# Performance work log

Measured on AMD Instinct MI355X. Metric: run time of the kernel, lower is better.

## Reference

```python
import jax, jax.numpy as jnp
import numpy as np
from jax import lax

T, B, NPG, F_IN = 10, 8, 1080, 2
N = B * NPG            # 8640 nodes total
DEG = 16
E = N * DEG            # 138240 edges
HID, HEADS = 64, 8
LSTM_H, OUT = 128, 2
NEG_SLOPE = 0.2

# (in_dim, heads, out_channels_per_head) for the 4 GATConv layers
LAYER_DIMS = [(F_IN, HEADS, HID), (HID * HEADS, HEADS, HID // 2),
              (HID // 2 * HEADS, HEADS, HID // 4), (HID // 4 * HEADS, 1, HID // 8)]


def setup_inputs() -> dict:
    key = jax.random.key(0)
    ks = iter(jax.random.split(key, 40))
    inp = {}
    inp['x_seq'] = jax.random.normal(next(ks), (T, N, F_IN), jnp.float32)
    # kNN-style edges within each graph: every node receives DEG random in-graph neighbors
    dst = jnp.repeat(jnp.arange(N, dtype=jnp.int32), DEG)
    offs = (dst // NPG) * NPG
    src = offs + jax.random.randint(next(ks), (E,), 0, NPG, jnp.int32)
    inp['edge_index'] = jnp.stack([src, dst])
    inp['batch'] = jnp.repeat(jnp.arange(B, dtype=jnp.int32), NPG)
    # GAT params: W [in, H*C], att_src/att_dst [H, C], bias [H*C]
    for li, (fin, h, c) in enumerate(LAYER_DIMS, start=1):
        s = 1.0 / np.sqrt(fin)
        inp[f'W{li}'] = jax.random.uniform(next(ks), (fin, h * c), jnp.float32, -s, s)
        inp[f'as{li}'] = jax.random.uniform(next(ks), (h, c), jnp.float32, -s, s)
        inp[f'ad{li}'] = jax.random.uniform(next(ks), (h, c), jnp.float32, -s, s)
        inp[f'b{li}'] = jnp.zeros((h * c,), jnp.float32)
    # LSTM (PyTorch layout, gate order i,f,g,o)
    gdim = HID // 8
    sl = 1.0 / np.sqrt(LSTM_H)
    inp['w_ih'] = jax.random.uniform(next(ks), (4 * LSTM_H, gdim), jnp.float32, -sl, sl)
    inp['w_hh'] = jax.random.uniform(next(ks), (4 * LSTM_H, LSTM_H), jnp.float32, -sl, sl)
    inp['b_ih'] = jax.random.uniform(next(ks), (4 * LSTM_H,), jnp.float32, -sl, sl)
    inp['b_hh'] = jax.random.uniform(next(ks), (4 * LSTM_H,), jnp.float32, -sl, sl)
    inp['w_fc'] = jax.random.uniform(next(ks), (OUT, LSTM_H), jnp.float32, -sl, sl)
    inp['b_fc'] = jax.random.uniform(next(ks), (OUT,), jnp.float32, -sl, sl)
    return inp


def _forward(x_seq, W1, as1, ad1, b1, W2, as2, ad2, b2, W3, as3, ad3, b3,
             W4, as4, ad4, b4, w_ih, w_hh, b_ih, b_hh, w_fc, b_fc,
             edge_index, batch):
    # PyG GATConv adds self-loops by default
    loops = jnp.arange(N, dtype=edge_index.dtype)
    src = jnp.concatenate([edge_index[0], loops])
    dst = jnp.concatenate([edge_index[1], loops])

    def gat(x, W, a_s, a_d, b):
        Hh, C = a_s.shape
        h = (x @ W).reshape(N, Hh, C)                 # [N,H,C]
        e_s = (h * a_s).sum(-1)                        # [N,H]
        e_d = (h * a_d).sum(-1)
        e = jax.nn.leaky_relu(e_s[src] + e_d[dst], NEG_SLOPE)   # [Etot,H]
        m = jax.ops.segment_max(e, dst, num_segments=N)
        ex = jnp.exp(e - m[dst])
        den = jax.ops.segment_sum(ex, dst, num_segments=N)
        alpha = ex / (den[dst] + 1e-16)
        out = jax.ops.segment_sum(h[src] * alpha[:, :, None], dst, num_segments=N)
        return out.reshape(N, Hh * C) + b

    counts = jax.ops.segment_sum(jnp.ones((N,), jnp.float32), batch, num_segments=B)[:, None]

    def per_t(x):  # eval mode: dropout = identity
        x = jax.nn.elu(gat(x, W1, as1, ad1, b1))
        x = jax.nn.elu(gat(x, W2, as2, ad2, b2))
        x = jax.nn.elu(gat(x, W3, as3, ad3, b3))
        x = jax.nn.elu(gat(x, W4, as4, ad4, b4))
        return jax.ops.segment_sum(x, batch, num_segments=B) / counts  # mean pool [B, hid//8]

    _, embs = lax.scan(lambda c, xt: (c, per_t(xt)), None, x_seq)  # [T,B,gdim]

    h0 = jnp.zeros((B, LSTM_H), x_seq.dtype)
    c0 = jnp.zeros((B, LSTM_H), x_seq.dtype)

    def step(carry, xt):
        h, c = carry
        g = xt @ w_ih.T + h @ w_hh.T + b_ih + b_hh
        i, f, gg, o = jnp.split(g, 4, axis=-1)
        c = jax.nn.sigmoid(f) * c + jax.nn.sigmoid(i) * jnp.tanh(gg)
        h = jax.nn.sigmoid(o) * jnp.tanh(c)
        return (h, c), None

    (h_last, _), _ = lax.scan(step, (h0, c0), embs)
    return h_last @ w_fc.T + b_fc  # [B, OUT] (eval path: last timestep only)


def reference(x_seq, W1, as1, ad1, b1, W2, as2, ad2, b2, W3, as3, ad3, b3,
              W4, as4, ad4, b4, w_ih, w_hh, b_ih, b_hh, w_fc, b_fc,
              edge_index, batch):
    return _forward(x_seq, W1, as1, ad1, b1, W2, as2, ad2, b2, W3, as3, ad3, b3,
                    W4, as4, ad4, b4, w_ih, w_hh, b_ih, b_hh, w_fc, b_fc,
                    edge_index, batch)
```

## Files before the change

kernel.cpp:

```cpp
#include <hip/hip_runtime.h>
#include <math.h>

#define T_TOT 10
#define NB    8
#define NPG   1080
#define NN    (NB*NPG)
#define DEG   16

typedef unsigned short ushortT;
using short8 = __attribute__((ext_vector_type(8))) short;
using f32x4  = __attribute__((ext_vector_type(4))) float;

__device__ __forceinline__ float lrelu(float v) { return v > 0.f ? v : 0.2f*v; }
__device__ __forceinline__ float elu1(float v)  { return v > 0.f ? v : (__expf(v) - 1.f); }
__device__ __forceinline__ float bf2f(ushortT h){ return __uint_as_float(((unsigned)h) << 16); }
__device__ __forceinline__ ushortT rne(float v) {
    unsigned u = __float_as_uint(v);
    u += 0x7FFFu + ((u >> 16) & 1u);
    return (ushortT)(u >> 16);
}
__device__ __forceinline__ int xswz(int b, int nwg) {
    int q = nwg >> 3, r = nwg & 7;
    int x = b & 7, i = b >> 3;
    return x*q + min(x, r) + i;
}

__global__ void k_prep_l1(const float* __restrict__ W1, const float* __restrict__ as1,
                          const float* __restrict__ ad1, float* __restrict__ A) {
    int tid = threadIdx.x;
    if (tid >= 32) return;
    int h = tid & 7, k = (tid >> 3) & 1, sd = tid >> 4;
    const float* att = sd ? ad1 : as1;
    float acc = 0.f;
    for (int c = 0; c < 64; ++c) acc += W1[k*512 + h*64 + c] * att[h*64 + c];
    A[sd*16 + k*8 + h] = acc;
}

__global__ void k_prepW(const float* __restrict__ W, ushortT* __restrict__ WT, int K, int M) {
    int i = blockIdx.x*256 + threadIdx.x;
    if (i >= K*M) return;
    int k = i / M, m = i - k*M;
    WT[(size_t)m*K + k] = rne(W[i]);
}

__global__ void k_e1(const float* __restrict__ x, const float* __restrict__ A,
                     float* __restrict__ es, float* __restrict__ ed, int R) {
    int r = blockIdx.x*256 + threadIdx.x;
    if (r >= R) return;
    float x0 = x[2*r], x1 = x[2*r+1];
    #pragma unroll
    for (int h = 0; h < 8; ++h) {
        es[r*8+h] = x0*A[h]    + x1*A[8+h];
        ed[r*8+h] = x0*A[16+h] + x1*A[24+h];
    }
}

__global__ __launch_bounds__(256) void k_gat1(
    const float* __restrict__ x, const int* __restrict__ esrc,
    const float* __restrict__ es, const float* __restrict__ ed,
    const float* __restrict__ W1, const float* __restrict__ b1,
    ushortT* __restrict__ q, int R) {
    int tid = threadIdx.x;
    int g = xswz(blockIdx.x, gridDim.x)*16 + (tid >> 4);
    int l = tid & 15;
    if (g >= R*8) g = R*8 - 1;
    int r = g >> 3, hh = g & 7;
    int t = r / NN, n = r - t*NN;
    float edv = ed[r*8 + hh];
    int s0 = t*NN + esrc[n*DEG + l];
    float e0 = lrelu(es[s0*8 + hh] + edv);
    float e1 = (l == 0) ? lrelu(es[r*8 + hh] + edv) : -1e30f;
    float m = fmaxf(e0, e1);
    #pragma unroll
    for (int off = 8; off >= 1; off >>= 1) m = fmaxf(m, __shfl_xor(m, off, 16));
    float ex0 = __expf(e0 - m);
    float ex1 = (l == 0) ? __expf(e1 - m) : 0.f;
    float den = ex0 + ex1;
    float p0 = ex0*x[2*s0]   + ex1*x[2*r];
    float p1 = ex0*x[2*s0+1] + ex1*x[2*r+1];
    #pragma unroll
    for (int off = 8; off >= 1; off >>= 1) {
        den += __shfl_xor(den, off, 16);
        p0  += __shfl_xor(p0,  off, 16);
        p1  += __shfl_xor(p1,  off, 16);
    }
    float inv = 1.f/(den + 1e-16f);
    float xa0 = p0*inv, xa1 = p1*inv;
    int col = hh*64 + l*4;
    float4 w0 = *(const float4*)&W1[col];
    float4 w1 = *(const float4*)&W1[512 + col];
    float4 bb = *(const float4*)&b1[col];
    ushort4 h4;
    h4.x = rne(elu1(xa0*w0.x + xa1*w1.x + bb.x));
    h4.y = rne(elu1(xa0*w0.y + xa1*w1.y + bb.y));
    h4.z = rne(elu1(xa0*w0.z + xa1*w1.z + bb.z));
    h4.w = rne(elu1(xa0*w0.w + xa1*w1.w + bb.w));
    *(ushort4*)&q[(size_t)r*512 + col] = h4;
}

template<int H, int C, bool BFIN, bool BFOUT>
__global__ __launch_bounds__(256) void k_gat(
    const void* __restrict__ hb_, const int* __restrict__ esrc,
    const float* __restrict__ es, const float* __restrict__ ed,
    const float* __restrict__ bias, float* __restrict__ out,
    ushortT* __restrict__ ohi, int R) {
    constexpr int LANES = C/4;
    constexpr int GPB = 256/LANES;
    constexpr int EPL = (17 + LANES - 1)/LANES;
    __shared__ float wsm[GPB][17];
    __shared__ int   ssm[GPB][17];
    int tid = threadIdx.x;
    int grp = tid / LANES;
    int l = tid % LANES;
    int g = xswz(blockIdx.x, gridDim.x)*GPB + grp;
    if (g >= R*H) g = R*H - 1;
    int r = g / H, hh = g % H;
    int t = r / NN, n = r - t*NN;
    float edv = ed[(size_t)r*H + hh];
    float ev[EPL]; int sv[EPL];
    float m = -1e30f;
    #pragma unroll
    for (int s = 0; s < EPL; ++s) {
        int j = s*LANES + l;
        if (j < 17) {
            int src = (j == 16) ? r : (t*NN + esrc[n*DEG + j]);
            sv[s] = src;
            float e = lrelu(es[(size_t)src*H + hh] + edv);
            ev[s] = e; m = fmaxf(m, e);
        } else { ev[s] = -1e30f; sv[s] = r; }
    }
    #pragma unroll
    for (int off = LANES/2; off >= 1; off >>= 1) m = fmaxf(m, __shfl_xor(m, off, LANES));
    float den = 0.f;
    #pragma unroll
    for (int s = 0; s < EPL; ++s) {
        int j = s*LANES + l;
        float e2 = (j < 17) ? __expf(ev[s] - m) : 0.f;
        ev[s] = e2; den += e2;
    }
    #pragma unroll
    for (int off = LANES/2; off >= 1; off >>= 1) den += __shfl_xor(den, off, LANES);
    float inv = 1.f/(den + 1e-16f);
    #pragma unroll
    for (int s = 0; s < EPL; ++s) {
        int j = s*LANES + l;
        if (j < 17) { wsm[grp][j] = ev[s]*inv; ssm[grp][j] = sv[s]; }
    }
    __syncthreads();
    constexpr int HC = H*C;
    int base = hh*C + l*4;
    float ax = 0.f, ay = 0.f, az = 0.f, aw = 0.f;
    #pragma unroll
    for (int j = 0; j < 17; ++j) {
        float wj = wsm[grp][j];
        if constexpr (BFIN) {
            ushort4 hv = *(const ushort4*)&((const ushortT*)hb_)[(size_t)ssm[grp][j]*HC + base];
            ax += wj*bf2f(hv.x); ay += wj*bf2f(hv.y); az += wj*bf2f(hv.z); aw += wj*bf2f(hv.w);
        } else {
            float4 hv = *(const float4*)&((const float*)hb_)[(size_t)ssm[grp][j]*HC + base];
            ax += wj*hv.x; ay += wj*hv.y; az += wj*hv.z; aw += wj*hv.w;
        }
    }
    float4 bb = *(const float4*)&bias[base];
    float vx = elu1(ax + bb.x), vy = elu1(ay + bb.y);
    float vz = elu1(az + bb.z), vw = elu1(aw + bb.w);
    if constexpr (BFOUT) {
        ushort4 h4;
        h4.x = rne(vx); h4.y = rne(vy); h4.z = rne(vz); h4.w = rne(vw);
        *(ushort4*)&ohi[(size_t)r*HC + base] = h4;
    } else {
        *(float4*)&out[(size_t)r*HC + base] = make_float4(vx, vy, vz, vw);
    }
}

template<int C>
__global__ __launch_bounds__(256) void k_gemm_mfma(
    const ushortT* __restrict__ X, const ushortT* __restrict__ WT,
    const float* __restrict__ as_, const float* __restrict__ ad_,
    ushortT* __restrict__ Hout, float* __restrict__ es, float* __restrict__ ed,
    int R, int K, int M) {
    __shared__ __align__(16) char smem[32768];
    int tid = threadIdx.x;
    int wid = tid >> 6, l = tid & 63;
    int l15 = l & 15, lg = l >> 4;
    int wr = wid >> 1, wc = wid & 1;
    int rb = blockIdx.x*128, cb = blockIdx.y*128;

    f32x4 acc[4][4] = {};
    int aoff[4], asw[4], boff[4], bsw[4];
    #pragma unroll
    for (int i = 0; i < 4; ++i) {
        int ar = wr*64 + i*16 + l15;
        aoff[i] = ar*128; asw[i] = (ar & 7) << 4;
        int bc = wc*64 + i*16 + l15;
        boff[i] = 16384 + bc*128; bsw[i] = (bc & 7) << 4;
    }
    int kb0 = lg*16;
    const size_t strideB = (size_t)K*2;
    int srow = tid >> 3, sc8 = tid & 7;
    int ssw = ((srow & 7) << 4);
    const int nKT = K >> 6;

    for (int kt = 0; kt < nKT; ++kt) {
        int kbyte = kt*128;
        __syncthreads();
        #pragma unroll
        for (int i = 0; i < 4; ++i) {
            int row = srow + i*32;
            int dst = row*128 + ((sc8*16) ^ ssw);
            int rg = min(rb + row, R - 1);
            uint4 va = *(const uint4*)((const char*)X  + (size_t)rg*strideB + kbyte + sc8*16);
            uint4 vw = *(const uint4*)((const char*)WT + (size_t)(cb + row)*strideB + kbyte + sc8*16);
            *(uint4*)(smem + dst)         = va;
            *(uint4*)(smem + 16384 + dst) = vw;
        }
        __syncthreads();
        #pragma unroll
        for (int ks = 0; ks < 2; ++ks) {
            int kb = ks*64 + kb0;
            short8 ah[4], bv[4];
            #pragma unroll
            for (int i = 0; i < 4; ++i) {
                ah[i] = *(const short8*)(smem + aoff[i] + (kb ^ asw[i]));
                bv[i] = *(const short8*)(smem + boff[i] + (kb ^ bsw[i]));
            }
            #pragma unroll
            for (int mt = 0; mt < 4; ++mt)
                #pragma unroll
                for (int nt = 0; nt < 4; ++nt)
                    acc[mt][nt] = __builtin_amdgcn_mfma_f32_16x16x32_bf16(ah[mt], bv[nt], acc[mt][nt], 0, 0, 0);
        }
    }
    __syncthreads();
    constexpr int NSL = 128/C;
    constexpr int NHW = 64/C;
    int hg0 = cb / C;
    float asv[4], adv[4];
    #pragma unroll
    for (int nt = 0; nt < 4; ++nt) {
        int col = wc*64 + nt*16 + l15;
        int h = col / C, c = col - h*C;
        asv[nt] = as_[(hg0 + h)*C + c];
        adv[nt] = ad_[(hg0 + h)*C + c];
    }
    float* ebp = (float*)smem;
    #pragma unroll
    for (int mt = 0; mt < 4; ++mt) {
        float ps[4][NHW] = {}, pd[4][NHW] = {};
        #pragma unroll
        for (int nt = 0; nt < 4; ++nt) {
            int sl = (nt*16)/C;
            #pragma unroll
            for (int q = 0; q < 4; ++q) {
                ps[q][sl] += acc[mt][nt][q]*asv[nt];
                pd[q][sl] += acc[mt][nt][q]*adv[nt];
            }
        }
        #pragma unroll
        for (int off = 1; off < 16; off <<= 1)
            #pragma unroll
            for (int q = 0; q < 4; ++q)
                #pragma unroll
                for (int sl = 0; sl < NHW; ++sl) {
                    ps[q][sl] += __shfl_xor(ps[q][sl], off);
                    pd[q][sl] += __shfl_xor(pd[q][sl], off);
                }
        if (l15 == 0) {
            #pragma unroll
            for (int q = 0; q < 4; ++q) {
                int row = wr*64 + mt*16 + lg*4 + q;
                #pragma unroll
                for (int sl = 0; sl < NHW; ++sl) {
                    ebp[(row*NSL + wc*NHW + sl)*2 + 0] = ps[q][sl];
                    ebp[(row*NSL + wc*NHW + sl)*2 + 1] = pd[q][sl];
                }
            }
        }
        #pragma unroll
        for (int nt = 0; nt < 4; ++nt) {
            int col = cb + wc*64 + nt*16 + l15;
            #pragma unroll
            for (int q = 0; q < 4; ++q) {
                int r = rb + wr*64 + mt*16 + lg*4 + q;
                if (r < R) Hout[(size_t)r*M + col] = rne(acc[mt][nt][q]);
            }
        }
    }
    __syncthreads();
    for (int i = tid; i < 128*NSL; i += 256) {
        int row = i / NSL, sl = i - row*NSL;
        int r = rb + row;
        if (r < R) {
            es[(size_t)r*8 + hg0 + sl] = ebp[i*2 + 0];
            ed[(size_t)r*8 + hg0 + sl] = ebp[i*2 + 1];
        }
    }
}

__global__ __launch_bounds__(256) void k_lin4(
    const float* __restrict__ X, const float* __restrict__ W,
    const float* __restrict__ as_, const float* __restrict__ ad_,
    float* __restrict__ Hout, float* __restrict__ es, float* __restrict__ ed, int R) {
    int tid = threadIdx.x;
    int lane = tid & 63;
    int rl = lane >> 3, cc = lane & 7;
    int r = blockIdx.x*32 + (tid >> 6)*8 + rl;
    if (r >= R) return;
    const float* xp = X + (size_t)r*128;
    float acc = 0.f;
    #pragma unroll 8
    for (int k = 0; k < 128; ++k) acc += xp[k] * W[k*8 + cc];
    Hout[(size_t)r*8 + cc] = acc;
    float ps = acc * as_[cc], pd = acc * ad_[cc];
    #pragma unroll
    for (int off = 4; off >= 1; off >>= 1) {
        ps += __shfl_xor(ps, off, 64);
        pd += __shfl_xor(pd, off, 64);
    }
    if (cc == 0) { es[r] = ps; ed[r] = pd; }
}

__global__ void k_pool(const float* __restrict__ x4, float* __restrict__ emb, int t0) {
    __shared__ float red[256];
    int tl = blockIdx.x >> 3, b = blockIdx.x & 7;
    int tid = threadIdx.x;
    int c = tid & 7, nl = tid >> 3;
    float s = 0.f;
    for (int k = 0; k < 34; ++k) {
        int n = nl + 32*k;
        if (n < NPG) s += x4[((size_t)tl*NN + b*NPG + n)*8 + c];
    }
    red[tid] = s;
    __syncthreads();
    for (int st = 16; st >= 1; st >>= 1) {
        if (nl < st) red[tid] += red[tid + st*8];
        __syncthreads();
    }
    if (nl == 0) emb[((t0 + tl)*8 + b)*8 + c] = red[c] * (1.f/1080.f);
}

__global__ __launch_bounds__(512) void k_lstm(
    const float* __restrict__ emb, const float* __restrict__ w_ih,
    const float* __restrict__ w_hh, const float* __restrict__ b_ih,
    const float* __restrict__ b_hh, const float* __restrict__ w_fc,
    const float* __restrict__ b_fc, float* __restrict__ out) {
    int b = blockIdx.x, u = threadIdx.x;
    __shared__ float h[128], cst[128], g[512], eall[T_TOT*8];
    if (u < 128) { h[u] = 0.f; cst[u] = 0.f; }
    if (u < T_TOT*8) eall[u] = emb[((u >> 3)*8 + b)*8 + (u & 7)];
    float wreg[128];
    {
        const float* wp = w_hh + (size_t)u*128;
        #pragma unroll
        for (int k4 = 0; k4 < 32; ++k4) {
            float4 v = *(const float4*)&wp[k4*4];
            wreg[4*k4+0] = v.x; wreg[4*k4+1] = v.y;
            wreg[4*k4+2] = v.z; wreg[4*k4+3] = v.w;
        }
    }
    float wih[8];
    #pragma unroll
    for (int k = 0; k < 8; ++k) wih[k] = w_ih[(size_t)u*8 + k];
    float bsum = b_ih[u] + b_hh[u];
    __syncthreads();
    for (int t = 0; t < T_TOT; ++t) {
        float a0 = bsum, a1 = 0.f, a2 = 0.f, a3 = 0.f;
        #pragma unroll
        for (int k = 0; k < 8; ++k) a0 += eall[t*8 + k]*wih[k];
        #pragma unroll
        for (int k = 0; k < 32; ++k) {
            a0 += h[4*k+0]*wreg[4*k+0];
            a1 += h[4*k+1]*wreg[4*k+1];
            a2 += h[4*k+2]*wreg[4*k+2];
            a3 += h[4*k+3]*wreg[4*k+3];
        }
        g[u] = (a0 + a1) + (a2 + a3);
        __syncthreads();
        if (u < 128) {
            float ig = 1.f/(1.f + __expf(-g[u]));
            float fg = 1.f/(1.f + __expf(-g[128+u]));
            float gg = tanhf(g[256+u]);
            float og = 1.f/(1.f + __expf(-g[384+u]));
            float cn = fg*cst[u] + ig*gg;
            cst[u] = cn;
            h[u] = og*tanhf(cn);
        }
        __syncthreads();
    }
    if (u < 64) {
        float p0 = h[u]*w_fc[u]       + h[u+64]*w_fc[64+u];
        float p1 = h[u]*w_fc[128+u]   + h[u+64]*w_fc[192+u];
        #pragma unroll
        for (int off = 32; off >= 1; off >>= 1) {
            p0 += __shfl_xor(p0, off, 64);
            p1 += __shfl_xor(p1, off, 64);
        }
        if (u == 0) {
            out[b*2 + 0] = p0 + b_fc[0];
            out[b*2 + 1] = p1 + b_fc[1];
        }
    }
}

extern "C" void kernel_launch(void* const* d_in, const int* in_sizes, int n_in,
                              void* d_out, int out_size, void* d_ws, size_t ws_size,
                              hipStream_t stream) {
    const float* x_seq = (const float*)d_in[0];
    const int*   edge  = (const int*)d_in[1];
    const float* W1 = (const float*)d_in[3];
    const float* as1 = (const float*)d_in[4];
    const float* ad1 = (const float*)d_in[5];
    const float* b1  = (const float*)d_in[6];
    const float* W2 = (const float*)d_in[7];
    const float* as2 = (const float*)d_in[8];
    const float* ad2 = (const float*)d_in[9];
    const float* b2  = (const float*)d_in[10];
    const float* W3 = (const float*)d_in[11];
    const float* as3 = (const float*)d_in[12];
    const float* ad3 = (const float*)d_in[13];
    const float* b3  = (const float*)d_in[14];
    const float* W4 = (const float*)d_in[15];
    const float* as4 = (const float*)d_in[16];
    const float* ad4 = (const float*)d_in[17];
    const float* b4  = (const float*)d_in[18];
    const float* w_ih = (const float*)d_in[19];
    const float* w_hh = (const float*)d_in[20];
    const float* b_ih = (const float*)d_in[21];
    const float* b_hh = (const float*)d_in[22];
    const float* w_fc = (const float*)d_in[23];
    const float* b_fc = (const float*)d_in[24];

    char* w = (char*)d_ws;
    auto alloc = [&](size_t bytes) {
        char* p = w; w += (bytes + 255) & ~(size_t)255; return p;
    };
    float*   A1  = (float*)alloc(128);
    float*   emb = (float*)alloc((size_t)T_TOT*8*8*4);
    ushortT* W2T = (ushortT*)alloc((size_t)256*512*2);
    ushortT* W3T = (ushortT*)alloc((size_t)128*256*2);
    size_t used = (size_t)(w - (char*)d_ws);
    size_t perT = (size_t)NN*(1024 + 512 + 512 + 256 + 512 + 128);
    size_t rem = (ws_size > used + 4096) ? ws_size - used - 4096 : 0;
    int Tc = (int)(rem / perT);
    if (Tc > T_TOT) Tc = T_TOT;
    if (Tc < 1) Tc = 1;
    ushortT* Q  = (ushortT*)alloc((size_t)Tc*NN*1024);
    ushortT* P  = (ushortT*)alloc((size_t)Tc*NN*512);
    ushortT* G3 = (ushortT*)alloc((size_t)Tc*NN*512);
    ushortT* H3 = (ushortT*)alloc((size_t)Tc*NN*256);
    float*   G4 = (float*)alloc((size_t)Tc*NN*512);
    float*   ES = (float*)alloc((size_t)Tc*NN*32);
    float*   ED = (float*)alloc((size_t)Tc*NN*32);
    float*   P4 = (float*)alloc((size_t)Tc*NN*32);
    float*   G5 = (float*)alloc((size_t)Tc*NN*32);

    k_prep_l1<<<1, 64, 0, stream>>>(W1, as1, ad1, A1);
    k_prepW<<<(256*512 + 255)/256, 256, 0, stream>>>(W2, W2T, 512, 256);
    k_prepW<<<(128*256 + 255)/256, 256, 0, stream>>>(W3, W3T, 256, 128);

    for (int t0 = 0; t0 < T_TOT; t0 += Tc) {
        int tc = (Tc < T_TOT - t0) ? Tc : (T_TOT - t0);
        int R = tc*NN;
        int nrb = (R + 127)/128;
        const float* xoff = x_seq + (size_t)t0*NN*2;
        k_e1<<<(R + 255)/256, 256, 0, stream>>>(xoff, A1, ES, ED, R);
        k_gat1<<<R/2, 256, 0, stream>>>(xoff, edge, ES, ED, W1, b1, Q, R);
        k_gemm_mfma<32><<<dim3(nrb, 2), 256, 0, stream>>>(Q, W2T, as2, ad2, P, ES, ED, R, 512, 256);
        k_gat<8,32,true,true><<<R/4, 256, 0, stream>>>(P, edge, ES, ED, b2, nullptr, G3, R);
        k_gemm_mfma<16><<<dim3(nrb, 1), 256, 0, stream>>>(G3, W3T, as3, ad3, H3, ES, ED, R, 256, 128);
        k_gat<8,16,true,false><<<R/8, 256, 0, stream>>>(H3, edge, ES, ED, b3, G4, nullptr, R);
        k_lin4<<<R/32, 256, 0, stream>>>(G4, W4, as4, ad4, P4, ES, ED, R);
        k_gat<1,8,false,false><<<(R + 127)/128, 256, 0, stream>>>(P4, edge, ES, ED, b4, G5, nullptr, R);
        k_pool<<<tc*8, 256, 0, stream>>>(G5, emb, t0);
    }
    k_lstm<<<8, 512, 0, stream>>>(emb, w_ih, w_hh, b_ih, b_hh, w_fc, b_fc, (float*)d_out);
}
```

Baseline: 437.8 us.

## Fuse layer-1 scores into gat1, widen per-lane gathers, store layer-3 output as bf16

```diff
diff --git a/kernel.cpp b/kernel.cpp
--- a/kernel.cpp
+++ b/kernel.cpp
@@ -14,10 +14,15 @@
 __device__ __forceinline__ float lrelu(float v) { return v > 0.f ? v : 0.2f*v; }
 __device__ __forceinline__ float elu1(float v)  { return v > 0.f ? v : (__expf(v) - 1.f); }
 __device__ __forceinline__ float bf2f(ushortT h){ return __uint_as_float(((unsigned)h) << 16); }
+__device__ __forceinline__ float bfl(unsigned u){ return __uint_as_float(u << 16); }
+__device__ __forceinline__ float bfh(unsigned u){ return __uint_as_float(u & 0xFFFF0000u); }
 __device__ __forceinline__ ushortT rne(float v) {
     unsigned u = __float_as_uint(v);
     u += 0x7FFFu + ((u >> 16) & 1u);
     return (ushortT)(u >> 16);
+}
+__device__ __forceinline__ unsigned pk2(float a, float b) {
+    return (unsigned)rne(a) | ((unsigned)rne(b) << 16);
 }
 __device__ __forceinline__ int xswz(int b, int nwg) {
     int q = nwg >> 3, r = nwg & 7;
@@ -43,76 +48,78 @@
     WT[(size_t)m*K + k] = rne(W[i]);
 }
 
-__global__ void k_e1(const float* __restrict__ x, const float* __restrict__ A,
-                     float* __restrict__ es, float* __restrict__ ed, int R) {
-    int r = blockIdx.x*256 + threadIdx.x;
-    if (r >= R) return;
-    float x0 = x[2*r], x1 = x[2*r+1];
-    #pragma unroll
-    for (int h = 0; h < 8; ++h) {
-        es[r*8+h] = x0*A[h]    + x1*A[8+h];
-        ed[r*8+h] = x0*A[16+h] + x1*A[24+h];
-    }
-}
-
 __global__ __launch_bounds__(256) void k_gat1(
     const float* __restrict__ x, const int* __restrict__ esrc,
-    const float* __restrict__ es, const float* __restrict__ ed,
-    const float* __restrict__ W1, const float* __restrict__ b1,
-    ushortT* __restrict__ q, int R) {
+    const float* __restrict__ A, const float* __restrict__ W1,
+    const float* __restrict__ b1, ushortT* __restrict__ q, int R) {
     int tid = threadIdx.x;
-    int g = xswz(blockIdx.x, gridDim.x)*16 + (tid >> 4);
-    int l = tid & 15;
+    int g = xswz(blockIdx.x, gridDim.x)*32 + (tid >> 3);
+    int l = tid & 7;
     if (g >= R*8) g = R*8 - 1;
     int r = g >> 3, hh = g & 7;
     int t = r / NN, n = r - t*NN;
-    float edv = ed[r*8 + hh];
-    int s0 = t*NN + esrc[n*DEG + l];
-    float e0 = lrelu(es[s0*8 + hh] + edv);
-    float e1 = (l == 0) ? lrelu(es[r*8 + hh] + edv) : -1e30f;
-    float m = fmaxf(e0, e1);
-    #pragma unroll
-    for (int off = 8; off >= 1; off >>= 1) m = fmaxf(m, __shfl_xor(m, off, 16));
-    float ex0 = __expf(e0 - m);
-    float ex1 = (l == 0) ? __expf(e1 - m) : 0.f;
-    float den = ex0 + ex1;
-    float p0 = ex0*x[2*s0]   + ex1*x[2*r];
-    float p1 = ex0*x[2*s0+1] + ex1*x[2*r+1];
-    #pragma unroll
-    for (int off = 8; off >= 1; off >>= 1) {
-        den += __shfl_xor(den, off, 16);
-        p0  += __shfl_xor(p0,  off, 16);
-        p1  += __shfl_xor(p1,  off, 16);
+    float2 xr = *(const float2*)&x[2*r];
+    float As0 = A[hh], As1 = A[8+hh];
+    float edv = xr.x*A[16+hh] + xr.y*A[24+hh];
+    float ev[3], xs0[3], xs1[3];
+    float m = -1e30f;
+    #pragma unroll
+    for (int s = 0; s < 3; ++s) {
+        int j = s*8 + l;
+        if (j < 17) {
+            int src = (j == 16) ? r : (t*NN + esrc[n*DEG + j]);
+            float2 xs = *(const float2*)&x[2*src];
+            xs0[s] = xs.x; xs1[s] = xs.y;
+            float e = lrelu(xs.x*As0 + xs.y*As1 + edv);
+            ev[s] = e; m = fmaxf(m, e);
+        } else { ev[s] = -1e30f; xs0[s] = 0.f; xs1[s] = 0.f; }
+    }
+    #pragma unroll
+    for (int off = 4; off >= 1; off >>= 1) m = fmaxf(m, __shfl_xor(m, off, 8));
+    float den = 0.f, p0 = 0.f, p1 = 0.f;
+    #pragma unroll
+    for (int s = 0; s < 3; ++s) {
+        float e2 = __expf(ev[s] - m);
+        den += e2; p0 += e2*xs0[s]; p1 += e2*xs1[s];
+    }
+    #pragma unroll
+    for (int off = 4; off >= 1; off >>= 1) {
+        den += __shfl_xor(den, off, 8);
+        p0  += __shfl_xor(p0,  off, 8);
+        p1  += __shfl_xor(p1,  off, 8);
     }
     float inv = 1.f/(den + 1e-16f);
     float xa0 = p0*inv, xa1 = p1*inv;
-    int col = hh*64 + l*4;
-    float4 w0 = *(const float4*)&W1[col];
-    float4 w1 = *(const float4*)&W1[512 + col];
-    float4 bb = *(const float4*)&b1[col];
-    ushort4 h4;
-    h4.x = rne(elu1(xa0*w0.x + xa1*w1.x + bb.x));
-    h4.y = rne(elu1(xa0*w0.y + xa1*w1.y + bb.y));
-    h4.z = rne(elu1(xa0*w0.z + xa1*w1.z + bb.z));
-    h4.w = rne(elu1(xa0*w0.w + xa1*w1.w + bb.w));
-    *(ushort4*)&q[(size_t)r*512 + col] = h4;
-}
-
-template<int H, int C, bool BFIN, bool BFOUT>
+    int col = hh*64 + l*8;
+    float4 w0a = *(const float4*)&W1[col],       w0b = *(const float4*)&W1[col+4];
+    float4 w1a = *(const float4*)&W1[512+col],   w1b = *(const float4*)&W1[512+col+4];
+    float4 bba = *(const float4*)&b1[col],       bbb = *(const float4*)&b1[col+4];
+    float v0 = elu1(xa0*w0a.x + xa1*w1a.x + bba.x);
+    float v1 = elu1(xa0*w0a.y + xa1*w1a.y + bba.y);
+    float v2 = elu1(xa0*w0a.z + xa1*w1a.z + bba.z);
+    float v3 = elu1(xa0*w0a.w + xa1*w1a.w + bba.w);
+    float v4 = elu1(xa0*w0b.x + xa1*w1b.x + bbb.x);
+    float v5 = elu1(xa0*w0b.y + xa1*w1b.y + bbb.y);
+    float v6 = elu1(xa0*w0b.z + xa1*w1b.z + bbb.z);
+    float v7 = elu1(xa0*w0b.w + xa1*w1b.w + bbb.w);
+    uint4 o;
+    o.x = pk2(v0,v1); o.y = pk2(v2,v3); o.z = pk2(v4,v5); o.w = pk2(v6,v7);
+    *(uint4*)&q[(size_t)r*512 + col] = o;
+}
+
+template<int H, int C, int LANES, bool BFIN, bool BFOUT>
 __global__ __launch_bounds__(256) void k_gat(
     const void* __restrict__ hb_, const int* __restrict__ esrc,
     const float* __restrict__ es, const float* __restrict__ ed,
     const float* __restrict__ bias, float* __restrict__ out,
     ushortT* __restrict__ ohi, int R) {
-    constexpr int LANES = C/4;
+    constexpr int CPL = C/LANES;
     constexpr int GPB = 256/LANES;
     constexpr int EPL = (17 + LANES - 1)/LANES;
-    __shared__ float wsm[GPB][17];
-    __shared__ int   ssm[GPB][17];
+    constexpr int HC = H*C;
     int tid = threadIdx.x;
-    int grp = tid / LANES;
-    int l = tid % LANES;
-    int g = xswz(blockIdx.x, gridDim.x)*GPB + grp;
+    int l = tid & (LANES-1);
+    int g = xswz(blockIdx.x, gridDim.x)*GPB + tid/LANES;
     if (g >= R*H) g = R*H - 1;
     int r = g / H, hh = g % H;
     int t = r / NN, n = r - t*NN;
@@ -132,44 +139,48 @@
     #pragma unroll
     for (int off = LANES/2; off >= 1; off >>= 1) m = fmaxf(m, __shfl_xor(m, off, LANES));
     float den = 0.f;
+    float wv[EPL];
     #pragma unroll
     for (int s = 0; s < EPL; ++s) {
-        int j = s*LANES + l;
-        float e2 = (j < 17) ? __expf(ev[s] - m) : 0.f;
-        ev[s] = e2; den += e2;
+        float e2 = __expf(ev[s] - m);
+        wv[s] = e2; den += e2;
     }
     #pragma unroll
     for (int off = LANES/2; off >= 1; off >>= 1) den += __shfl_xor(den, off, LANES);
     float inv = 1.f/(den + 1e-16f);
     #pragma unroll
-    for (int s = 0; s < EPL; ++s) {
-        int j = s*LANES + l;
-        if (j < 17) { wsm[grp][j] = ev[s]*inv; ssm[grp][j] = sv[s]; }
-    }
-    __syncthreads();
-    constexpr int HC = H*C;
-    int base = hh*C + l*4;
-    float ax = 0.f, ay = 0.f, az = 0.f, aw = 0.f;
+    for (int s = 0; s < EPL; ++s) wv[s] *= inv;
+
+    int lb = (tid & 63) & ~(LANES-1);
+    float acc[CPL] = {};
     #pragma unroll
     for (int j = 0; j < 17; ++j) {
-        float wj = wsm[grp][j];
+        float wj = __shfl(wv[j/LANES], lb + (j & (LANES-1)), 64);
+        int   sj = __shfl(sv[j/LANES], lb + (j & (LANES-1)), 64);
         if constexpr (BFIN) {
-            ushort4 hv = *(const ushort4*)&((const ushortT*)hb_)[(size_t)ssm[grp][j]*HC + base];
-            ax += wj*bf2f(hv.x); ay += wj*bf2f(hv.y); az += wj*bf2f(hv.z); aw += wj*bf2f(hv.w);
+            const ushortT* hp = (const ushortT*)hb_ + (size_t)sj*HC + hh*C + l*CPL;
+            uint4 hv = *(const uint4*)hp;
+            acc[0] += wj*bfl(hv.x); acc[1] += wj*bfh(hv.x);
+            acc[2] += wj*bfl(hv.y); acc[3] += wj*bfh(hv.y);
+            acc[4] += wj*bfl(hv.z); acc[5] += wj*bfh(hv.z);
+            acc[6] += wj*bfl(hv.w); acc[7] += wj*bfh(hv.w);
         } else {
-            float4 hv = *(const float4*)&((const float*)hb_)[(size_t)ssm[grp][j]*HC + base];
-            ax += wj*hv.x; ay += wj*hv.y; az += wj*hv.z; aw += wj*hv.w;
-        }
-    }
-    float4 bb = *(const float4*)&bias[base];
-    float vx = elu1(ax + bb.x), vy = elu1(ay + bb.y);
-    float vz = elu1(az + bb.z), vw = elu1(aw + bb.w);
+            const float* hp = (const float*)hb_ + (size_t)sj*HC + hh*C + l*CPL;
+            float4 hv = *(const float4*)hp;
+            acc[0] += wj*hv.x; acc[1] += wj*hv.y;
+            acc[2] += wj*hv.z; acc[3] += wj*hv.w;
+        }
+    }
+    int base = hh*C + l*CPL;
+    #pragma unroll
+    for (int c = 0; c < CPL; ++c) acc[c] = elu1(acc[c] + bias[base + c]);
     if constexpr (BFOUT) {
-        ushort4 h4;
-        h4.x = rne(vx); h4.y = rne(vy); h4.z = rne(vz); h4.w = rne(vw);
-        *(ushort4*)&ohi[(size_t)r*HC + base] = h4;
+        uint4 o;
+        o.x = pk2(acc[0],acc[1]); o.y = pk2(acc[2],acc[3]);
+        o.z = pk2(acc[4],acc[5]); o.w = pk2(acc[6],acc[7]);
+        *(uint4*)&ohi[(size_t)r*HC + base] = o;
     } else {
-        *(float4*)&out[(size_t)r*HC + base] = make_float4(vx, vy, vz, vw);
+        *(float4*)&out[(size_t)r*HC + base] = make_float4(acc[0],acc[1],acc[2],acc[3]);
     }
 }
 
@@ -298,26 +309,43 @@
 }
 
 __global__ __launch_bounds__(256) void k_lin4(
-    const float* __restrict__ X, const float* __restrict__ W,
+    const ushortT* __restrict__ X, const float* __restrict__ W,
     const float* __restrict__ as_, const float* __restrict__ ad_,
     float* __restrict__ Hout, float* __restrict__ es, float* __restrict__ ed, int R) {
     int tid = threadIdx.x;
-    int lane = tid & 63;
-    int rl = lane >> 3, cc = lane & 7;
-    int r = blockIdx.x*32 + (tid >> 6)*8 + rl;
+    int l = tid & 7;
+    int r = blockIdx.x*32 + (tid >> 3);
     if (r >= R) return;
-    const float* xp = X + (size_t)r*128;
-    float acc = 0.f;
-    #pragma unroll 8
-    for (int k = 0; k < 128; ++k) acc += xp[k] * W[k*8 + cc];
-    Hout[(size_t)r*8 + cc] = acc;
-    float ps = acc * as_[cc], pd = acc * ad_[cc];
-    #pragma unroll
-    for (int off = 4; off >= 1; off >>= 1) {
-        ps += __shfl_xor(ps, off, 64);
-        pd += __shfl_xor(pd, off, 64);
-    }
-    if (cc == 0) { es[r] = ps; ed[r] = pd; }
+    const ushortT* xp = X + (size_t)r*128 + l*16;
+    uint4 a = *(const uint4*)xp;
+    uint4 b = *(const uint4*)(xp + 8);
+    float xv[16];
+    xv[0]=bfl(a.x); xv[1]=bfh(a.x); xv[2]=bfl(a.y); xv[3]=bfh(a.y);
+    xv[4]=bfl(a.z); xv[5]=bfh(a.z); xv[6]=bfl(a.w); xv[7]=bfh(a.w);
+    xv[8]=bfl(b.x); xv[9]=bfh(b.x); xv[10]=bfl(b.y); xv[11]=bfh(b.y);
+    xv[12]=bfl(b.z); xv[13]=bfh(b.z); xv[14]=bfl(b.w); xv[15]=bfh(b.w);
+    float acc[8] = {};
+    #pragma unroll
+    for (int kk = 0; kk < 16; ++kk) {
+        const float* wr = W + (l*16 + kk)*8;
+        float4 wa = *(const float4*)wr, wb = *(const float4*)(wr + 4);
+        acc[0] += xv[kk]*wa.x; acc[1] += xv[kk]*wa.y;
+        acc[2] += xv[kk]*wa.z; acc[3] += xv[kk]*wa.w;
+        acc[4] += xv[kk]*wb.x; acc[5] += xv[kk]*wb.y;
+        acc[6] += xv[kk]*wb.z; acc[7] += xv[kk]*wb.w;
+    }
+    #pragma unroll
+    for (int off = 4; off >= 1; off >>= 1)
+        #pragma unroll
+        for (int c = 0; c < 8; ++c) acc[c] += __shfl_xor(acc[c], off, 8);
+    if (l == 0) {
+        *(float4*)&Hout[(size_t)r*8]     = make_float4(acc[0],acc[1],acc[2],acc[3]);
+        *(float4*)&Hout[(size_t)r*8 + 4] = make_float4(acc[4],acc[5],acc[6],acc[7]);
+        float ps = 0.f, pd = 0.f;
+        #pragma unroll
+        for (int c = 0; c < 8; ++c) { ps += acc[c]*as_[c]; pd += acc[c]*ad_[c]; }
+        es[r] = ps; ed[r] = pd;
+    }
 }
 
 __global__ void k_pool(const float* __restrict__ x4, float* __restrict__ emb, int t0) {
@@ -439,7 +467,7 @@
     ushortT* W2T = (ushortT*)alloc((size_t)256*512*2);
     ushortT* W3T = (ushortT*)alloc((size_t)128*256*2);
     size_t used = (size_t)(w - (char*)d_ws);
-    size_t perT = (size_t)NN*(1024 + 512 + 512 + 256 + 512 + 128);
+    size_t perT = (size_t)NN*(1024 + 512 + 512 + 256 + 256 + 128);
     size_t rem = (ws_size > used + 4096) ? ws_size - used - 4096 : 0;
     int Tc = (int)(rem / perT);
     if (Tc > T_TOT) Tc = T_TOT;
@@ -448,7 +476,7 @@
     ushortT* P  = (ushortT*)alloc((size_t)Tc*NN*512);
     ushortT* G3 = (ushortT*)alloc((size_t)Tc*NN*512);
     ushortT* H3 = (ushortT*)alloc((size_t)Tc*NN*256);
-    float*   G4 = (float*)alloc((size_t)Tc*NN*512);
+    ushortT* G4 = (ushortT*)alloc((size_t)Tc*NN*256);
     float*   ES = (float*)alloc((size_t)Tc*NN*32);
     float*   ED = (float*)alloc((size_t)Tc*NN*32);
     float*   P4 = (float*)alloc((size_t)Tc*NN*32);
@@ -463,14 +491,13 @@
         int R = tc*NN;
         int nrb = (R + 127)/128;
         const float* xoff = x_seq + (size_t)t0*NN*2;
-        k_e1<<<(R + 255)/256, 256, 0, stream>>>(xoff, A1, ES, ED, R);
-        k_gat1<<<R/2, 256, 0, stream>>>(xoff, edge, ES, ED, W1, b1, Q, R);
+        k_gat1<<<(R*8 + 31)/32, 256, 0, stream>>>(xoff, edge, A1, W1, b1, Q, R);
         k_gemm_mfma<32><<<dim3(nrb, 2), 256, 0, stream>>>(Q, W2T, as2, ad2, P, ES, ED, R, 512, 256);
-        k_gat<8,32,true,true><<<R/4, 256, 0, stream>>>(P, edge, ES, ED, b2, nullptr, G3, R);
+        k_gat<8,32,4,true,true><<<(R*8 + 63)/64, 256, 0, stream>>>(P, edge, ES, ED, b2, nullptr, G3, R);
         k_gemm_mfma<16><<<dim3(nrb, 1), 256, 0, stream>>>(G3, W3T, as3, ad3, H3, ES, ED, R, 256, 128);
-        k_gat<8,16,true,false><<<R/8, 256, 0, stream>>>(H3, edge, ES, ED, b3, G4, nullptr, R);
-        k_lin4<<<R/32, 256, 0, stream>>>(G4, W4, as4, ad4, P4, ES, ED, R);
-        k_gat<1,8,false,false><<<(R + 127)/128, 256, 0, stream>>>(P4, edge, ES, ED, b4, G5, nullptr, R);
+        k_gat<8,16,2,true,true><<<(R*8 + 127)/128, 256, 0, stream>>>(H3, edge, ES, ED, b3, nullptr, G4, R);
+        k_lin4<<<(R + 31)/32, 256, 0, stream>>>(G4, W4, as4, ad4, P4, ES, ED, R);
+        k_gat<1,8,2,false,false><<<(R + 127)/128, 256, 0, stream>>>(P4, edge, ES, ED, b4, G5, nullptr, R);
         k_pool<<<tc*8, 256, 0, stream>>>(G5, emb, t0);
     }
     k_lstm<<<8, 512, 0, stream>>>(emb, w_ih, w_hh, b_ih, b_hh, w_fc, b_fc, (float*)d_out);
```

Result: faster. 400.6 us (-8.5%).
